# Kernel tuning notes

Measured on AMD Instinct MI355X. Metric: run time of the kernel, lower is better.

## Reference

```python
import jax, jax.numpy as jnp
import numpy as np

N = 100000       # node_num / batch_node_num
E = 1_600_000    # edges (avg degree 16)
IN_DIM = 256
OUT_DIM = 128
SLOPE = 0.1


def setup_inputs() -> dict:
    key = jax.random.key(0)
    k0, k1, k2, k3, k4 = jax.random.split(key, 5)
    node_feats = jax.random.normal(k0, (N, IN_DIM), jnp.float32)
    W = jax.random.normal(k1, (OUT_DIM, IN_DIM), jnp.float32) * (1.0 / np.sqrt(IN_DIM))
    b = jnp.zeros((OUT_DIM,), jnp.float32)
    # a ~ kaiming_normal for shape [2*out_dim, 1]; stored flat here
    a = jax.random.normal(k2, (2 * OUT_DIM,), jnp.float32) * np.sqrt(2.0 / (2 * OUT_DIM))
    src = jax.random.randint(k3, (E,), 0, N, dtype=jnp.int32)
    dst = jax.random.randint(k4, (E,), 0, N, dtype=jnp.int32)
    return {"node_feats": node_feats, "W": W, "b": b, "a": a, "src": src, "dst": dst}


def reference(node_feats, W, b, a, src, dst):
    n = node_feats.shape[0]
    d = W.shape[0]
    # out_linear_layer
    emb = node_feats @ W.T + b                      # [N, D]
    # append self-loop edges (original_node_edge)
    loop = jnp.arange(n, dtype=src.dtype)
    s = jnp.concatenate([src, loop])                # [E+N]
    t = jnp.concatenate([dst, loop])                # [E+N]
    # concat(emb[s], emb[t]) @ a  ==  emb[s] @ a[:D] + emb[t] @ a[D:]
    logits = emb[s] @ a[:d] + emb[t] @ a[d:]        # [E+N]
    score = jnp.exp(jax.nn.leaky_relu(logits, negative_slope=SLOPE))
    # sparse.mm(matrix, emb) and sparse.mm(matrix, ones): segment sums over src rows
    num = jax.ops.segment_sum(score[:, None] * emb[t], s, num_segments=n)  # [N, D]
    den = jax.ops.segment_sum(score, s, num_segments=n)                    # [N]
    return num / den[:, None]
```

## Files before the change

kernel.cpp:

```cpp
#include <hip/hip_runtime.h>
#include <hip/hip_bf16.h>

#define IN_DIM 256
#define OUT_DIM 128
#define SLOPE 0.1f

#define BM 128
#define BN 128
#define BK 32

__global__ __launch_bounds__(256) void gemm_kernel(
    const float* __restrict__ A,
    const float* __restrict__ W,
    const float* __restrict__ bias,
    const float* __restrict__ avec,
    float* __restrict__ emb,
    float* __restrict__ a1,
    float* __restrict__ a2,
    int N) {
  __shared__ float As[BM][BK + 1];
  __shared__ float Bs[BK][BN + 4];

  const int tid = threadIdx.x;
  const int row0 = blockIdx.x * BM;
  const int tx = tid & 15;
  const int ty = tid >> 4;

  float acc[8][8] = {};

  for (int k0 = 0; k0 < IN_DIM; k0 += BK) {
#pragma unroll
    for (int i = 0; i < 4; ++i) {
      int f = tid + i * 256;
      int r = f >> 3;
      int c4 = (f & 7) * 4;
      float4 v = make_float4(0.f, 0.f, 0.f, 0.f);
      if (row0 + r < N)
        v = *(const float4*)&A[(size_t)(row0 + r) * IN_DIM + k0 + c4];
      As[r][c4 + 0] = v.x; As[r][c4 + 1] = v.y;
      As[r][c4 + 2] = v.z; As[r][c4 + 3] = v.w;
    }
#pragma unroll
    for (int i = 0; i < 4; ++i) {
      int f = tid + i * 256;
      int nn = f >> 3;
      int c4 = (f & 7) * 4;
      float4 v = *(const float4*)&W[(size_t)nn * IN_DIM + k0 + c4];
      Bs[c4 + 0][nn] = v.x; Bs[c4 + 1][nn] = v.y;
      Bs[c4 + 2][nn] = v.z; Bs[c4 + 3][nn] = v.w;
    }
    __syncthreads();

#pragma unroll
    for (int k = 0; k < BK; ++k) {
      float a_[8], b_[8];
#pragma unroll
      for (int j = 0; j < 8; ++j) a_[j] = As[ty * 8 + j][k];
#pragma unroll
      for (int i = 0; i < 8; ++i) b_[i] = Bs[k][tx * 8 + i];
#pragma unroll
      for (int j = 0; j < 8; ++j)
#pragma unroll
        for (int i = 0; i < 8; ++i) acc[j][i] += a_[j] * b_[i];
    }
    __syncthreads();
  }

  float p1[8], p2[8];
#pragma unroll
  for (int j = 0; j < 8; ++j) { p1[j] = 0.f; p2[j] = 0.f; }

#pragma unroll
  for (int j = 0; j < 8; ++j) {
    int r = row0 + ty * 8 + j;
    if (r < N) {
#pragma unroll
      for (int i = 0; i < 8; i += 4) {
        int c = tx * 8 + i;
        float4 v;
        v.x = acc[j][i + 0] + bias[c + 0];
        v.y = acc[j][i + 1] + bias[c + 1];
        v.z = acc[j][i + 2] + bias[c + 2];
        v.w = acc[j][i + 3] + bias[c + 3];
        *(float4*)&emb[(size_t)r * OUT_DIM + c] = v;
        p1[j] += v.x * avec[c + 0] + v.y * avec[c + 1] +
                 v.z * avec[c + 2] + v.w * avec[c + 3];
        p2[j] += v.x * avec[OUT_DIM + c + 0] + v.y * avec[OUT_DIM + c + 1] +
                 v.z * avec[OUT_DIM + c + 2] + v.w * avec[OUT_DIM + c + 3];
      }
    }
  }
#pragma unroll
  for (int j = 0; j < 8; ++j) {
#pragma unroll
    for (int d = 1; d < 16; d <<= 1) {
      p1[j] += __shfl_xor(p1[j], d, 64);
      p2[j] += __shfl_xor(p2[j], d, 64);
    }
  }
  if (tx == 0) {
#pragma unroll
    for (int j = 0; j < 8; ++j) {
      int r = row0 + ty * 8 + j;
      if (r < N) { a1[r] = p1[j]; a2[r] = p2[j]; }
    }
  }
}

__global__ void hist_kernel(const int* __restrict__ src, int* __restrict__ deg,
                            int E) {
  int i = blockIdx.x * blockDim.x + threadIdx.x;
  if (i < E) atomicAdd(&deg[src[i]], 1);
}

__global__ __launch_bounds__(1024) void scan1_kernel(
    const int* __restrict__ deg, int* __restrict__ offset,
    int* __restrict__ blocksum, int N) {
  __shared__ int tmp[16];
  const int tid = threadIdx.x;
  const int lane = tid & 63;
  const int wave = tid >> 6;
  int i = blockIdx.x * 1024 + tid;
  int v = (i < N) ? deg[i] : 0;
  int x = v;
#pragma unroll
  for (int d = 1; d < 64; d <<= 1) {
    int y = __shfl_up(x, d, 64);
    if (lane >= d) x += y;
  }
  if (lane == 63) tmp[wave] = x;
  __syncthreads();
  if (tid < 16) {
    int wv = tmp[tid];
#pragma unroll
    for (int d = 1; d < 16; d <<= 1) {
      int y = __shfl_up(wv, d, 16);
      if (tid >= d) wv += y;
    }
    tmp[tid] = wv;
  }
  __syncthreads();
  int waveoff = (wave == 0) ? 0 : tmp[wave - 1];
  if (i < N) offset[i] = waveoff + x - v;
  if (tid == 0) blocksum[blockIdx.x] = tmp[15];
}

__global__ __launch_bounds__(1024) void scan2_kernel(int* __restrict__ blocksum,
                                                     int nb) {
  __shared__ int tmp[16];
  const int tid = threadIdx.x;
  const int lane = tid & 63;
  const int wave = tid >> 6;
  int v = (tid < nb) ? blocksum[tid] : 0;
  int x = v;
#pragma unroll
  for (int d = 1; d < 64; d <<= 1) {
    int y = __shfl_up(x, d, 64);
    if (lane >= d) x += y;
  }
  if (lane == 63) tmp[wave] = x;
  __syncthreads();
  if (tid < 16) {
    int wv = tmp[tid];
#pragma unroll
    for (int d = 1; d < 16; d <<= 1) {
      int y = __shfl_up(wv, d, 16);
      if (tid >= d) wv += y;
    }
    tmp[tid] = wv;
  }
  __syncthreads();
  int waveoff = (wave == 0) ? 0 : tmp[wave - 1];
  if (tid < nb) blocksum[tid] = waveoff + x - v;
}

__global__ void scan3_kernel(int* __restrict__ offset,
                             const int* __restrict__ blocksum,
                             int* __restrict__ pos, int N) {
  int i = blockIdx.x * blockDim.x + threadIdx.x;
  if (i < N) {
    int o = offset[i] + blocksum[i >> 10];
    offset[i] = o;
    pos[i] = o;
  }
}

__global__ void scatter_kernel(const int* __restrict__ src,
                               const int* __restrict__ dst,
                               int* __restrict__ pos,
                               int* __restrict__ tsorted, int E) {
  int i = blockIdx.x * blockDim.x + threadIdx.x;
  if (i < E) {
    int p = atomicAdd(&pos[src[i]], 1);
    tsorted[p] = dst[i];
  }
}

__global__ __launch_bounds__(256) void aggregate_kernel(
    const float* __restrict__ emb, const float* __restrict__ a1,
    const float* __restrict__ a2, const int* __restrict__ offset,
    const int* __restrict__ deg, const int* __restrict__ tsorted,
    float* __restrict__ out, int N) {
  int n = (int)((blockIdx.x * (size_t)blockDim.x + threadIdx.x) >> 6);
  int lane = threadIdx.x & 63;
  if (n >= N) return;
  const int half = lane >> 5;
  const int sub = lane & 31;

  const float as = a1[n];
  const int beg = offset[n];
  const int cnt = deg[n];
  const int items = cnt + 1;
  const int niter = (items + 1) >> 1;

  float4 acc = make_float4(0.f, 0.f, 0.f, 0.f);
  float den = 0.f;

  int idx = half;
  int t = (idx == 0 || idx > cnt) ? n : tsorted[beg + idx - 1];
  float at = a2[t];

  for (int i = 0; i < niter; ++i) {
    const bool valid = (idx < items);
    const float4 v = *(const float4*)&emb[(size_t)t * OUT_DIM + sub * 4];
    const float logit = as + at;
    int idxn = idx + 2;
    if (i + 1 < niter) {
      int tn = (idxn <= cnt) ? tsorted[beg + idxn - 1] : n;
      t = tn;
      at = a2[tn];
    }
    idx = idxn;
    float sc = valid ? __expf(logit > 0.f ? logit : SLOPE * logit) : 0.f;
    acc.x += sc * v.x;
    acc.y += sc * v.y;
    acc.z += sc * v.z;
    acc.w += sc * v.w;
    den += sc;
  }

  acc.x += __shfl_xor(acc.x, 32, 64);
  acc.y += __shfl_xor(acc.y, 32, 64);
  acc.z += __shfl_xor(acc.z, 32, 64);
  acc.w += __shfl_xor(acc.w, 32, 64);
  den   += __shfl_xor(den,   32, 64);

  if (half == 0) {
    const float inv = 1.0f / den;
    float4 o = make_float4(acc.x * inv, acc.y * inv, acc.z * inv, acc.w * inv);
    *(float4*)&out[(size_t)n * OUT_DIM + sub * 4] = o;
  }
}

extern "C" void kernel_launch(void* const* d_in, const int* in_sizes, int n_in,
                              void* d_out, int out_size, void* d_ws,
                              size_t ws_size, hipStream_t stream) {
  const float* node_feats = (const float*)d_in[0];
  const float* W = (const float*)d_in[1];
  const float* bias = (const float*)d_in[2];
  const float* avec = (const float*)d_in[3];
  const int* src = (const int*)d_in[4];
  const int* dst = (const int*)d_in[5];
  float* out = (float*)d_out;

  const int OUT = in_sizes[2];
  const int IN = in_sizes[1] / OUT;
  const int N = in_sizes[0] / IN;
  const int E = in_sizes[4];
  const int NB = (N + 1023) / 1024;

  char* p = (char*)d_ws;
  auto alloc = [&](size_t bytes) {
    void* r = (void*)p;
    p += (bytes + 255) & ~(size_t)255;
    return r;
  };
  float* emb = (float*)alloc((size_t)N * OUT * sizeof(float));
  float* a1 = (float*)alloc((size_t)N * sizeof(float));
  float* a2 = (float*)alloc((size_t)N * sizeof(float));
  int* deg = (int*)alloc((size_t)N * sizeof(int));
  int* offset = (int*)alloc((size_t)N * sizeof(int));
  int* pos = (int*)alloc((size_t)N * sizeof(int));
  int* blocksum = (int*)alloc((size_t)NB * sizeof(int));
  int* tsorted = (int*)alloc((size_t)E * sizeof(int));

  hipMemsetAsync(deg, 0, (size_t)N * sizeof(int), stream);

  hist_kernel<<<(E + 255) / 256, 256, 0, stream>>>(src, deg, E);

  gemm_kernel<<<(N + BM - 1) / BM, 256, 0, stream>>>(
      node_feats, W, bias, avec, emb, a1, a2, N);

  scan1_kernel<<<NB, 1024, 0, stream>>>(deg, offset, blocksum, N);
  scan2_kernel<<<1, 1024, 0, stream>>>(blocksum, NB);
  scan3_kernel<<<(N + 255) / 256, 256, 0, stream>>>(offset, blocksum, pos, N);

  scatter_kernel<<<(E + 255) / 256, 256, 0, stream>>>(src, dst, pos, tsorted,
                                                      E);

  aggregate_kernel<<<(N + 3) / 4, 256, 0, stream>>>(emb, a1, a2, offset, deg,
                                                    tsorted, out, N);
}
```

Measured before the change: 600.9 us.

## Use split-bf16 MFMA for the linear layer and widen aggregate gather to 4 edges

The FP32 SIMT GEMM is replaced with a matrix-core kernel that splits A and W into hi/lo bf16 parts and accumulates three bf16 MFMA products to approximate FP32 accuracy. W is converted once per call in a small pre-kernel, and A is split on the fly in registers. The aggregate kernel now processes four edges per iteration (16 lanes each, 8 floats per lane) to raise memory-level parallelism on the gather. The split-bf16 scheme drops the lo*lo term, which slightly reduces precision. W reads come straight from global memory without shared-memory staging, and each wave re-reads W.

```diff
diff --git a/kernel.cpp b/kernel.cpp
--- a/kernel.cpp
+++ b/kernel.cpp
@@ -5,104 +5,100 @@
 #define OUT_DIM 128
 #define SLOPE 0.1f
 
-#define BM 128
-#define BN 128
-#define BK 32
-
-__global__ __launch_bounds__(256) void gemm_kernel(
+typedef __attribute__((ext_vector_type(8))) __bf16 bf16x8;
+typedef __attribute__((ext_vector_type(4))) float f32x4;
+
+__global__ void convert_w_kernel(const float* __restrict__ W,
+                                 __bf16* __restrict__ Whi,
+                                 __bf16* __restrict__ Wlo, int total) {
+  int i = blockIdx.x * blockDim.x + threadIdx.x;
+  if (i < total) {
+    float x = W[i];
+    __bf16 h = (__bf16)x;
+    __bf16 l = (__bf16)(x - (float)h);
+    Whi[i] = h;
+    Wlo[i] = l;
+  }
+}
+
+__global__ __launch_bounds__(256) void gemm_mfma_kernel(
     const float* __restrict__ A,
-    const float* __restrict__ W,
+    const __bf16* __restrict__ Whi,
+    const __bf16* __restrict__ Wlo,
     const float* __restrict__ bias,
     const float* __restrict__ avec,
     float* __restrict__ emb,
     float* __restrict__ a1,
     float* __restrict__ a2,
     int N) {
-  __shared__ float As[BM][BK + 1];
-  __shared__ float Bs[BK][BN + 4];
-
-  const int tid = threadIdx.x;
-  const int row0 = blockIdx.x * BM;
-  const int tx = tid & 15;
-  const int ty = tid >> 4;
-
-  float acc[8][8] = {};
-
-  for (int k0 = 0; k0 < IN_DIM; k0 += BK) {
-#pragma unroll
-    for (int i = 0; i < 4; ++i) {
-      int f = tid + i * 256;
-      int r = f >> 3;
-      int c4 = (f & 7) * 4;
-      float4 v = make_float4(0.f, 0.f, 0.f, 0.f);
-      if (row0 + r < N)
-        v = *(const float4*)&A[(size_t)(row0 + r) * IN_DIM + k0 + c4];
-      As[r][c4 + 0] = v.x; As[r][c4 + 1] = v.y;
-      As[r][c4 + 2] = v.z; As[r][c4 + 3] = v.w;
-    }
-#pragma unroll
-    for (int i = 0; i < 4; ++i) {
-      int f = tid + i * 256;
-      int nn = f >> 3;
-      int c4 = (f & 7) * 4;
-      float4 v = *(const float4*)&W[(size_t)nn * IN_DIM + k0 + c4];
-      Bs[c4 + 0][nn] = v.x; Bs[c4 + 1][nn] = v.y;
-      Bs[c4 + 2][nn] = v.z; Bs[c4 + 3][nn] = v.w;
-    }
-    __syncthreads();
-
-#pragma unroll
-    for (int k = 0; k < BK; ++k) {
-      float a_[8], b_[8];
-#pragma unroll
-      for (int j = 0; j < 8; ++j) a_[j] = As[ty * 8 + j][k];
-#pragma unroll
-      for (int i = 0; i < 8; ++i) b_[i] = Bs[k][tx * 8 + i];
-#pragma unroll
-      for (int j = 0; j < 8; ++j)
-#pragma unroll
-        for (int i = 0; i < 8; ++i) acc[j][i] += a_[j] * b_[i];
-    }
-    __syncthreads();
-  }
-
-  float p1[8], p2[8];
-#pragma unroll
-  for (int j = 0; j < 8; ++j) { p1[j] = 0.f; p2[j] = 0.f; }
-
-#pragma unroll
-  for (int j = 0; j < 8; ++j) {
-    int r = row0 + ty * 8 + j;
-    if (r < N) {
-#pragma unroll
-      for (int i = 0; i < 8; i += 4) {
-        int c = tx * 8 + i;
-        float4 v;
-        v.x = acc[j][i + 0] + bias[c + 0];
-        v.y = acc[j][i + 1] + bias[c + 1];
-        v.z = acc[j][i + 2] + bias[c + 2];
-        v.w = acc[j][i + 3] + bias[c + 3];
-        *(float4*)&emb[(size_t)r * OUT_DIM + c] = v;
-        p1[j] += v.x * avec[c + 0] + v.y * avec[c + 1] +
-                 v.z * avec[c + 2] + v.w * avec[c + 3];
-        p2[j] += v.x * avec[OUT_DIM + c + 0] + v.y * avec[OUT_DIM + c + 1] +
-                 v.z * avec[OUT_DIM + c + 2] + v.w * avec[OUT_DIM + c + 3];
-      }
-    }
-  }
-#pragma unroll
-  for (int j = 0; j < 8; ++j) {
+  const int lane = threadIdx.x & 63;
+  const int wave = threadIdx.x >> 6;
+  const int m0 = blockIdx.x * 64 + wave * 16;
+  const int lr = lane & 15;
+  const int lg = lane >> 4;
+
+  int arow = m0 + lr;
+  if (arow > N - 1) arow = N - 1;
+  const float* aptr = A + (size_t)arow * IN_DIM + lg * 8;
+
+  f32x4 acc[8];
+#pragma unroll
+  for (int t = 0; t < 8; ++t) acc[t] = (f32x4)(0.f);
+
+  for (int k0 = 0; k0 < IN_DIM; k0 += 32) {
+    float4 q0 = *(const float4*)(aptr + k0);
+    float4 q1 = *(const float4*)(aptr + k0 + 4);
+    float qs[8] = {q0.x, q0.y, q0.z, q0.w, q1.x, q1.y, q1.z, q1.w};
+    bf16x8 ahi, alo;
+#pragma unroll
+    for (int j = 0; j < 8; ++j) {
+      float x = qs[j];
+      __bf16 h = (__bf16)x;
+      ahi[j] = h;
+      alo[j] = (__bf16)(x - (float)h);
+    }
+    const int kcol = k0 + lg * 8;
+#pragma unroll
+    for (int t = 0; t < 8; ++t) {
+      const size_t woff = (size_t)(t * 16 + lr) * IN_DIM + kcol;
+      bf16x8 bhi = *(const bf16x8*)(Whi + woff);
+      bf16x8 blo = *(const bf16x8*)(Wlo + woff);
+      acc[t] = __builtin_amdgcn_mfma_f32_16x16x32_bf16(ahi, bhi, acc[t], 0, 0, 0);
+      acc[t] = __builtin_amdgcn_mfma_f32_16x16x32_bf16(ahi, blo, acc[t], 0, 0, 0);
+      acc[t] = __builtin_amdgcn_mfma_f32_16x16x32_bf16(alo, bhi, acc[t], 0, 0, 0);
+    }
+  }
+
+  float p1[4] = {0.f, 0.f, 0.f, 0.f};
+  float p2[4] = {0.f, 0.f, 0.f, 0.f};
+#pragma unroll
+  for (int t = 0; t < 8; ++t) {
+    const int c = t * 16 + lr;
+    const float bv = bias[c];
+    const float av1 = avec[c];
+    const float av2 = avec[OUT_DIM + c];
+#pragma unroll
+    for (int v = 0; v < 4; ++v) {
+      const int r = m0 + lg * 4 + v;
+      const float e = acc[t][v] + bv;
+      if (r < N) emb[(size_t)r * OUT_DIM + c] = e;
+      p1[v] += e * av1;
+      p2[v] += e * av2;
+    }
+  }
+#pragma unroll
+  for (int v = 0; v < 4; ++v) {
 #pragma unroll
     for (int d = 1; d < 16; d <<= 1) {
-      p1[j] += __shfl_xor(p1[j], d, 64);
-      p2[j] += __shfl_xor(p2[j], d, 64);
-    }
-  }
-  if (tx == 0) {
-#pragma unroll
-    for (int j = 0; j < 8; ++j) {
-      int r = row0 + ty * 8 + j;
-      if (r < N) { a1[r] = p1[j]; a2[r] = p2[j]; }
+      p1[v] += __shfl_xor(p1[v], d, 64);
+      p2[v] += __shfl_xor(p2[v], d, 64);
+    }
+  }
+  if (lr == 0) {
+#pragma unroll
+    for (int v = 0; v < 4; ++v) {
+      const int r = m0 + lg * 4 + v;
+      if (r < N) { a1[r] = p1[v]; a2[r] = p2[v]; }
     }
   }
 }
@@ -204,51 +200,64 @@
   int n = (int)((blockIdx.x * (size_t)blockDim.x + threadIdx.x) >> 6);
   int lane = threadIdx.x & 63;
   if (n >= N) return;
-  const int half = lane >> 5;
-  const int sub = lane & 31;
+  const int q = lane >> 4;
+  const int sub = lane & 15;
 
   const float as = a1[n];
   const int beg = offset[n];
   const int cnt = deg[n];
   const int items = cnt + 1;
-  const int niter = (items + 1) >> 1;
-
-  float4 acc = make_float4(0.f, 0.f, 0.f, 0.f);
+  const int niter = (items + 3) >> 2;
+
+  float4 acc0 = make_float4(0.f, 0.f, 0.f, 0.f);
+  float4 acc1 = make_float4(0.f, 0.f, 0.f, 0.f);
   float den = 0.f;
 
-  int idx = half;
+  int idx = q;
   int t = (idx == 0 || idx > cnt) ? n : tsorted[beg + idx - 1];
   float at = a2[t];
 
   for (int i = 0; i < niter; ++i) {
     const bool valid = (idx < items);
-    const float4 v = *(const float4*)&emb[(size_t)t * OUT_DIM + sub * 4];
+    const float* row = emb + (size_t)t * OUT_DIM + sub * 8;
+    const float4 v0 = *(const float4*)row;
+    const float4 v1 = *(const float4*)(row + 4);
     const float logit = as + at;
-    int idxn = idx + 2;
+    const int idxn = idx + 4;
     if (i + 1 < niter) {
       int tn = (idxn <= cnt) ? tsorted[beg + idxn - 1] : n;
       t = tn;
       at = a2[tn];
     }
     idx = idxn;
-    float sc = valid ? __expf(logit > 0.f ? logit : SLOPE * logit) : 0.f;
-    acc.x += sc * v.x;
-    acc.y += sc * v.y;
-    acc.z += sc * v.z;
-    acc.w += sc * v.w;
+    const float sc = valid ? __expf(logit > 0.f ? logit : SLOPE * logit) : 0.f;
+    acc0.x += sc * v0.x; acc0.y += sc * v0.y;
+    acc0.z += sc * v0.z; acc0.w += sc * v0.w;
+    acc1.x += sc * v1.x; acc1.y += sc * v1.y;
+    acc1.z += sc * v1.z; acc1.w += sc * v1.w;
     den += sc;
   }
 
-  acc.x += __shfl_xor(acc.x, 32, 64);
-  acc.y += __shfl_xor(acc.y, 32, 64);
-  acc.z += __shfl_xor(acc.z, 32, 64);
-  acc.w += __shfl_xor(acc.w, 32, 64);
-  den   += __shfl_xor(den,   32, 64);
-
-  if (half == 0) {
+#pragma unroll
+  for (int d = 16; d < 64; d <<= 1) {
+    acc0.x += __shfl_xor(acc0.x, d, 64);
+    acc0.y += __shfl_xor(acc0.y, d, 64);
+    acc0.z += __shfl_xor(acc0.z, d, 64);
+    acc0.w += __shfl_xor(acc0.w, d, 64);
+    acc1.x += __shfl_xor(acc1.x, d, 64);
+    acc1.y += __shfl_xor(acc1.y, d, 64);
+    acc1.z += __shfl_xor(acc1.z, d, 64);
+    acc1.w += __shfl_xor(acc1.w, d, 64);
+    den    += __shfl_xor(den,    d, 64);
+  }
+
+  if (q == 0) {
     const float inv = 1.0f / den;
-    float4 o = make_float4(acc.x * inv, acc.y * inv, acc.z * inv, acc.w * inv);
-    *(float4*)&out[(size_t)n * OUT_DIM + sub * 4] = o;
+    float* op = out + (size_t)n * OUT_DIM + sub * 8;
+    *(float4*)op = make_float4(acc0.x * inv, acc0.y * inv, acc0.z * inv,
+                               acc0.w * inv);
+    *(float4*)(op + 4) = make_float4(acc1.x * inv, acc1.y * inv, acc1.z * inv,
+                                     acc1.w * inv);
   }
 }
 
@@ -268,6 +277,7 @@
   const int N = in_sizes[0] / IN;
   const int E = in_sizes[4];
   const int NB = (N + 1023) / 1024;
+  const int WTOT = in_sizes[1];
 
   char* p = (char*)d_ws;
   auto alloc = [&](size_t bytes) {
@@ -283,13 +293,16 @@
   int* pos = (int*)alloc((size_t)N * sizeof(int));
   int* blocksum = (int*)alloc((size_t)NB * sizeof(int));
   int* tsorted = (int*)alloc((size_t)E * sizeof(int));
+  __bf16* Whi = (__bf16*)alloc((size_t)WTOT * sizeof(__bf16));
+  __bf16* Wlo = (__bf16*)alloc((size_t)WTOT * sizeof(__bf16));
 
   hipMemsetAsync(deg, 0, (size_t)N * sizeof(int), stream);
 
+  convert_w_kernel<<<(WTOT + 255) / 256, 256, 0, stream>>>(W, Whi, Wlo, WTOT);
   hist_kernel<<<(E + 255) / 256, 256, 0, stream>>>(src, deg, E);
 
-  gemm_kernel<<<(N + BM - 1) / BM, 256, 0, stream>>>(
-      node_feats, W, bias, avec, emb, a1, a2, N);
+  gemm_mfma_kernel<<<(N + 63) / 64, 256, 0, stream>>>(
+      node_feats, Whi, Wlo, bias, avec, emb, a1, a2, N);
 
   scan1_kernel<<<NB, 1024, 0, stream>>>(deg, offset, blocksum, N);
   scan2_kernel<<<1, 1024, 0, stream>>>(blocksum, NB);
```

After: 580.5 us. 1.04x faster.
